# Kernel tuning notes

Hardware: AMD Instinct MI355X
Metric: run time of the kernel (lower is better)

## Reference

```python
import jax, jax.numpy as jnp
import numpy as np

N_EMBD = 1024
N_HEAD = 16
HEAD_DIM = N_EMBD // N_HEAD

def setup_inputs() -> dict:
    key = jax.random.key(0)
    ks = jax.random.split(key, 5)
    B, T, C = 2, 2048, N_EMBD
    s = 1.0 / np.sqrt(C)
    x = jax.random.normal(ks[0], (B, T, C), dtype=jnp.float32)
    W_qkv = jax.random.normal(ks[1], (C, 3 * C), dtype=jnp.float32) * s
    b_qkv = jax.random.normal(ks[2], (3 * C,), dtype=jnp.float32) * 0.02
    W_o = jax.random.normal(ks[3], (C, C), dtype=jnp.float32) * s
    b_o = jax.random.normal(ks[4], (C,), dtype=jnp.float32) * 0.02
    return {"x": x, "W_qkv": W_qkv, "b_qkv": b_qkv, "W_o": W_o, "b_o": b_o}

def reference(x, W_qkv, b_qkv, W_o, b_o):
    B, T, C = x.shape
    H, D = N_HEAD, HEAD_DIM
    scale = 1.0 / np.sqrt(D)
    qkv = jnp.einsum('btc,cf->btf', x, W_qkv) + b_qkv  # [B,T,3C]
    q, k, v = jnp.split(qkv, 3, axis=-1)
    # [B,H,T,D]
    q = q.reshape(B, T, H, D).transpose(0, 2, 1, 3)
    k = k.reshape(B, T, H, D).transpose(0, 2, 1, 3)
    v = v.reshape(B, T, H, D).transpose(0, 2, 1, 3)
    att = jnp.einsum('bhqd,bhkd->bhqk', q, k) * scale  # [B,H,T,T]
    causal = jnp.tril(jnp.ones((T, T), dtype=bool))
    att = jnp.where(causal[None, None], att, -jnp.inf)
    att = jax.nn.softmax(att, axis=-1)
    y = jnp.einsum('bhqk,bhkd->bhqd', att, v)  # [B,H,T,D]
    y = y.transpose(0, 2, 1, 3).reshape(B, T, C)
    return jnp.einsum('btc,cf->btf', y, W_o) + b_o
```

## Files before the change

### kernel.cpp

```cpp
#include <hip/hip_runtime.h>
#include <hip/hip_bf16.h>

#define TT 2048
#define BB 2
#define CC 1024
#define NH 16
#define HD 64

typedef __attribute__((ext_vector_type(8))) short short8;
typedef __attribute__((ext_vector_type(4))) short short4b;
typedef __attribute__((ext_vector_type(4))) float f32x4;

typedef unsigned int __attribute__((address_space(1))) ui_gas;
typedef unsigned int __attribute__((address_space(3))) ui_las;

#if __has_builtin(__builtin_amdgcn_mfma_f32_16x16x16bf16_1k)
#define PV16 1
#define VSS 4
#else
#define PV16 0
#define VSS 8
#endif

__device__ __forceinline__ float us2f(unsigned short u) {
    union { unsigned int i; float f; } v; v.i = ((unsigned int)u) << 16; return v.f;
}
__device__ __forceinline__ unsigned short f2us(float f) {
    union { float f; unsigned int i; } v; v.f = f;
    unsigned int i = v.i;
    unsigned int lsb = (i >> 16) & 1u;
    i += 0x7fffu + lsb;
    return (unsigned short)(i >> 16);
}
__device__ __forceinline__ unsigned int pack2_trunc(float a, float b) {
    union { float f; unsigned int u; } x, y; x.f = a; y.f = b;
    return (y.u & 0xffff0000u) | (x.u >> 16);
}

__device__ __forceinline__ void gl_lds16(const unsigned short* g, unsigned short* l) {
    __builtin_amdgcn_global_load_lds((const ui_gas*)g, (ui_las*)l, 16, 0, 0);
}

__device__ __forceinline__ float4 load4(const void* p, size_t i, int isbf) {
    if (isbf) {
        ushort4 u = *reinterpret_cast<const ushort4*>((const unsigned short*)p + i);
        return make_float4(us2f(u.x), us2f(u.y), us2f(u.z), us2f(u.w));
    } else {
        return *reinterpret_cast<const float4*>((const float*)p + i);
    }
}
__device__ __forceinline__ float load1(const void* p, size_t i, int isbf) {
    return isbf ? us2f(((const unsigned short*)p)[i]) : ((const float*)p)[i];
}

__global__ __launch_bounds__(256) void prep_kernel(
    const void* __restrict__ x, const void* __restrict__ Wqkv, const void* __restrict__ Wo,
    const void* __restrict__ bqkv, const void* __restrict__ bo,
    unsigned short* __restrict__ xb, unsigned short* __restrict__ Wqkvt,
    unsigned short* __restrict__ Wot, int* __restrict__ flags)
{
    __shared__ float Ls[64 * 65];
    __shared__ int sh_isbf;
    const int t = threadIdx.x;
    const int bid = blockIdx.x;

    const void* src;
    int mode, sub;
    if (bid < 2048)      { mode = 0; sub = bid;        src = x; }
    else if (bid < 2816) { mode = 1; sub = bid - 2048; src = Wqkv; }
    else                 { mode = 2; sub = bid - 2816; src = Wo; }

    if (bid == 0 && t < 64) {
        const void* ps[5] = {x, Wqkv, bqkv, Wo, bo};
        for (int k = 0; k < 5; ++k) {
            const unsigned short* u = (const unsigned short*)ps[k];
            int bad = 0;
            #pragma unroll
            for (int j = 0; j < 4; ++j) {
                float v = us2f(u[t * 4 + j]);
                if (!(fabsf(v) < 1e4f)) bad = 1;
            }
            unsigned long long m = __ballot(bad != 0);
            if (t == 0) flags[k] = (__popcll(m) < 4) ? 1 : 0;
        }
    }
    if (t < 64) {
        const unsigned short* u = (const unsigned short*)src;
        int bad = 0;
        #pragma unroll
        for (int j = 0; j < 4; ++j) {
            float v = us2f(u[t * 4 + j]);
            if (!(fabsf(v) < 1e4f)) bad = 1;
        }
        unsigned long long m = __ballot(bad != 0);
        if (t == 0) sh_isbf = (__popcll(m) < 4) ? 1 : 0;
    }
    __syncthreads();
    const int isbf = sh_isbf;

    if (mode == 0) {
        const size_t i = ((size_t)sub * 256 + t) * 8;
        float4 a = load4(src, i, isbf);
        float4 b = load4(src, i + 4, isbf);
        alignas(16) unsigned short pk[8];
        pk[0] = f2us(a.x); pk[1] = f2us(a.y); pk[2] = f2us(a.z); pk[3] = f2us(a.w);
        pk[4] = f2us(b.x); pk[5] = f2us(b.y); pk[6] = f2us(b.z); pk[7] = f2us(b.w);
        *reinterpret_cast<uint4*>(xb + i) = *reinterpret_cast<const uint4*>(pk);
        return;
    }

    int N, Krows, n0, k0;
    unsigned short* dst;
    if (mode == 1) { N = 3 * CC; Krows = CC; dst = Wqkvt; n0 = (sub % 48) * 64; k0 = (sub / 48) * 64; }
    else           { N = CC;     Krows = CC; dst = Wot;   n0 = (sub % 16) * 64; k0 = (sub / 16) * 64; }
    {
        const int r = t >> 2, cq = (t & 3) << 4;
        #pragma unroll
        for (int i = 0; i < 4; ++i) {
            float4 v = load4(src, (size_t)(k0 + r) * N + n0 + cq + i * 4, isbf);
            Ls[r * 65 + cq + i * 4 + 0] = v.x;
            Ls[r * 65 + cq + i * 4 + 1] = v.y;
            Ls[r * 65 + cq + i * 4 + 2] = v.z;
            Ls[r * 65 + cq + i * 4 + 3] = v.w;
        }
    }
    __syncthreads();
    {
        const int c = t & 63, kg = (t >> 6) * 16;
        alignas(16) unsigned short pk[16];
        #pragma unroll
        for (int i = 0; i < 16; ++i) pk[i] = f2us(Ls[(kg + i) * 65 + c]);
        unsigned short* d = dst + (size_t)(n0 + c) * Krows + k0 + kg;
        *reinterpret_cast<uint4*>(d + 0) = *reinterpret_cast<const uint4*>(&pk[0]);
        *reinterpret_cast<uint4*>(d + 8) = *reinterpret_cast<const uint4*>(&pk[8]);
    }
}

template<int WM, int WN, int NWM, int NWN, int SWZ, bool VTE>
__global__ __launch_bounds__(256) void gemm_mfma(
    const unsigned short* __restrict__ A,
    const unsigned short* __restrict__ Bt,
    const void* __restrict__ bias, void* __restrict__ C,
    unsigned short* __restrict__ Vt,
    int M, int N, int K,
    const int* __restrict__ flags, int biasfi, int cfi)
{
    constexpr int BM = WM * 16 * NWM, BN = WN * 16 * NWN;
    constexpr int ASL = BM / 16, BSL = BN / 16;
    constexpr int TOT = ASL + BSL;
    constexpr int PW  = TOT / 4;

    __shared__ __align__(16) unsigned short SH[3][TOT * 512];

    const int tid = threadIdx.x;
    const int l  = tid & 63;
    const int w  = tid >> 6;
    const int wm = w / NWN, wn = w % NWN;
    const int lm = l & 15;
    const int lk = (l >> 4) * 8;
    const int quad = l >> 4;

    int bx, by;
    if constexpr (SWZ == 1) {
        const int lin = blockIdx.y * 24 + blockIdx.x;
        const int xcd = lin & 7, loc = lin >> 3;
        bx = (xcd & 1) * 12 + loc % 12;
        by = (xcd >> 1) * 8 + loc / 12;
    } else if constexpr (SWZ == 2) {
        const int lin = blockIdx.y * 16 + blockIdx.x;
        const int xcd = lin & 7, loc = lin >> 3;
        bx = (xcd & 1) * 8 + (loc & 7);
        by = (xcd >> 1) * 16 + (loc >> 3);
    } else {
        bx = blockIdx.x; by = blockIdx.y;
    }
    const int bm = by * BM, bn = bx * BN;

    f32x4 acc[WM][WN];
    #pragma unroll
    for (int i = 0; i < WM; ++i)
        #pragma unroll
        for (int j = 0; j < WN; ++j) acc[i][j] = (f32x4){0.f, 0.f, 0.f, 0.f};

    auto stage = [&](int bb, int k0) {
        #pragma unroll
        for (int s = 0; s < PW; ++s) {
            const int slab = w * PW + s;
            const unsigned short* src;
            if (slab < ASL) src = A  + (size_t)(bm + slab * 16 + lm) * K + k0 + lk;
            else            src = Bt + (size_t)(bn + (slab - ASL) * 16 + lm) * K + k0 + lk;
            gl_lds16(src, &SH[bb][slab * 512]);
        }
    };

    auto compute = [&](int bb) {
        short8 af[WM], bf[WN];
        #pragma unroll
        for (int i = 0; i < WM; ++i)
            af[i] = *reinterpret_cast<const short8*>(&SH[bb][(wm * WM + i) * 512 + l * 8]);
        #pragma unroll
        for (int j = 0; j < WN; ++j)
            bf[j] = *reinterpret_cast<const short8*>(&SH[bb][(ASL + wn * WN + j) * 512 + l * 8]);
        #pragma unroll
        for (int i = 0; i < WM; ++i)
            #pragma unroll
            for (int j = 0; j < WN; ++j)
                acc[i][j] = __builtin_amdgcn_mfma_f32_16x16x32_bf16(af[i], bf[j], acc[i][j], 0, 0, 0);
    };

    const int nt = K >> 5;
    stage(0, 0);
    stage(1, 32);
    asm volatile("s_waitcnt vmcnt(%0)" :: "n"(PW) : "memory");
    __builtin_amdgcn_sched_barrier(0);
    __builtin_amdgcn_s_barrier();

    for (int t = 0; t < nt; ++t) {
        if (t + 2 < nt) stage((t + 2) % 3, (t + 2) << 5);
        compute(t % 3);
        if (t + 2 < nt) {
            asm volatile("s_waitcnt vmcnt(%0)" :: "n"(PW) : "memory");
        } else {
            asm volatile("s_waitcnt vmcnt(0)" ::: "memory");
        }
        __builtin_amdgcn_sched_barrier(0);
        __builtin_amdgcn_s_barrier();
    }

    const int bias_bf = (biasfi >= 0) ? flags[biasfi] : 0;
    const int c_bf    = (cfi >= 0) ? flags[cfi] : ((cfi == -2) ? 1 : 0);
    float bv[WN];
    #pragma unroll
    for (int j = 0; j < WN; ++j) bv[j] = load1(bias, bn + (WN * wn + j) * 16 + lm, bias_bf);

    constexpr int TS = BM + 8;
    unsigned short* FL = &SH[0][0];
    const bool vblk = VTE && (bn >= 2 * CC);

    #pragma unroll
    for (int i = 0; i < WM; ++i) {
        #pragma unroll
        for (int r = 0; r < 4; ++r) {
            const int rl = (WM * wm + i) * 16 + quad * 4 + r;
            const int row = bm + rl;
            #pragma unroll
            for (int j = 0; j < WN; ++j) {
                const int cl2 = (WN * wn + j) * 16 + lm;
                const int col = bn + cl2;
                const float val = acc[i][j][r] + bv[j];
                if (c_bf) {
                    const unsigned short us = f2us(val);
                    ((unsigned short*)C)[(size_t)row * N + col] = us;
                    if (vblk) FL[cl2 * TS + rl] = us;
                } else {
                    ((float*)C)[(size_t)row * N + col] = val;
                }
            }
        }
    }

    if constexpr (VTE) {
        static_assert(!VTE || (BM == 128 && BN % 64 == 0), "VTE geometry");
        static_assert(!VTE || (BN * (BM + 8) <= 3 * TOT * 512), "VTE LDS overlay");
        if (vblk) {
            __syncthreads();
            const int cl = tid >> 1, rq = tid & 1;
            const int cc2 = bn - 2 * CC + cl;
            const int hh = cc2 >> 6, dd = cc2 & 63;
            const int bq = bm >> 11;
            const int tk = (bm & (TT - 1)) + rq * 64;
            unsigned short* dst = Vt + ((size_t)(bq * NH + hh) * HD + dd) * TT + tk;
            const unsigned short* srcp = &FL[cl * TS + rq * 64];
            #pragma unroll
            for (int k = 0; k < 8; ++k)
                *(uint4*)(dst + k * 8) = *(const uint4*)(srcp + k * 8);
        }
    }
}

__global__ __launch_bounds__(256) void attn_mfma(
    const unsigned short* __restrict__ qkv,
    const unsigned short* __restrict__ Vt,
    unsigned short* __restrict__ y)
{
    __shared__ __align__(16) unsigned short Ksh[8 * 512];
    __shared__ __align__(16) unsigned short Vsh[1039 * VSS];

    const int tid = threadIdx.x;
    const int l   = tid & 63;
    const int w   = tid >> 6;
    const int quad = l >> 4;
    const int col  = l & 15;

    const int n  = blockIdx.x;
    const int g  = n >> 3;
    const int bh = (n & 7) * 4 + (g & 3);
    const int i  = g >> 2;
    const int tA = i, tB = 31 - i;
    const int b  = bh >> 4, h = bh & 15;

#if !PV16
    for (int ss = tid; ss < 1039; ss += 256)
        *(uint2*)(&Vsh[ss * 8 + 4]) = make_uint2(0u, 0u);
#endif

    const float QSCALE = 0.18033688f;
    short8 qfA[2], qfB[2];
    #pragma unroll
    for (int t2 = 0; t2 < 2; ++t2) {
        const int qt = t2 ? tB : tA;
        short8* qf = t2 ? qfB : qfA;
        const int token = qt * 64 + w * 16 + col;
        const unsigned short* qrow = qkv + (size_t)(b * TT + token) * 3 * CC + h * HD;
        #pragma unroll
        for (int ks = 0; ks < 2; ++ks) {
            ushort4 u0 = *(const ushort4*)(qrow + ks * 32 + quad * 8);
            ushort4 u1 = *(const ushort4*)(qrow + ks * 32 + quad * 8 + 4);
            alignas(16) unsigned short pk[8];
            pk[0] = f2us(us2f(u0.x) * QSCALE);
            pk[1] = f2us(us2f(u0.y) * QSCALE);
            pk[2] = f2us(us2f(u0.z) * QSCALE);
            pk[3] = f2us(us2f(u0.w) * QSCALE);
            pk[4] = f2us(us2f(u1.x) * QSCALE);
            pk[5] = f2us(us2f(u1.y) * QSCALE);
            pk[6] = f2us(us2f(u1.z) * QSCALE);
            pk[7] = f2us(us2f(u1.w) * QSCALE);
            qf[ks] = *(const short8*)pk;
        }
    }

    f32x4 oA[4], oB[4];
    #pragma unroll
    for (int nb = 0; nb < 4; ++nb) {
        oA[nb] = (f32x4){0.f, 0.f, 0.f, 0.f};
        oB[nb] = (f32x4){0.f, 0.f, 0.f, 0.f};
    }
    float lAc = 0.f, lBc = 0.f;

    const unsigned short* kbase = qkv + (size_t)b * TT * 3 * CC + CC + h * HD;
    const unsigned short* vbase = Vt + (size_t)bh * HD * TT;

    const int vd = tid >> 2, vg0 = (tid & 3) * 4;

    uint4 rk[2], rv[2];
    auto issue_loads = [&](int kt) {
        const unsigned short* ksrc = kbase + (size_t)(kt * 64 + l) * 3 * CC;
        #pragma unroll
        for (int c2 = 0; c2 < 2; ++c2) {
            const int c = 2 * w + c2;
            rk[c2] = *(const uint4*)(ksrc + c * 8);
        }
        const unsigned short* vsrc = vbase + (size_t)vd * TT + kt * 64 + vg0 * 4;
        rv[0] = *(const uint4*)(vsrc + 0);
        rv[1] = *(const uint4*)(vsrc + 8);
    };
    auto write_lds = [&]() {
        #pragma unroll
        for (int c2 = 0; c2 < 2; ++c2) {
            const int c = 2 * w + c2;
            const int ks = c >> 2, q = c & 3;
            const int slot = ((quad * 2 + ks) * 64 + q * 16 + col) * 8;
            *(uint4*)(&Ksh[slot]) = rk[c2];
        }
        *(uint2*)(&Vsh[((vg0 + 0) * 65 + vd) * VSS]) = make_uint2(rv[0].x, rv[0].y);
        *(uint2*)(&Vsh[((vg0 + 1) * 65 + vd) * VSS]) = make_uint2(rv[0].z, rv[0].w);
        *(uint2*)(&Vsh[((vg0 + 2) * 65 + vd) * VSS]) = make_uint2(rv[1].x, rv[1].y);
        *(uint2*)(&Vsh[((vg0 + 3) * 65 + vd) * VSS]) = make_uint2(rv[1].z, rv[1].w);
    };

    auto step = [&](const short8* qf, f32x4* o, float& l_i, bool diag) {
        f32x4 st[4];
        #pragma unroll
        for (int nb = 0; nb < 4; ++nb) {
            f32x4 acc = {0.f, 0.f, 0.f, 0.f};
            #pragma unroll
            for (int ks = 0; ks < 2; ++ks) {
                short8 kf = *(const short8*)(&Ksh[((nb * 2 + ks) * 64 + l) * 8]);
                acc = __builtin_amdgcn_mfma_f32_16x16x32_bf16(kf, qf[ks], acc, 0, 0, 0);
            }
            st[nb] = acc;
        }
        float pv[4][4];
        float rs = 0.f;
        #pragma unroll
        for (int nb = 0; nb < 4; ++nb)
            #pragma unroll
            for (int r = 0; r < 4; ++r) {
                float v = st[nb][r];
                if (diag && (nb * 16 + quad * 4 + r > w * 16 + col)) v = -3e38f;
                float p = __builtin_exp2f(v);
                pv[nb][r] = p;
                rs += p;
            }
        rs += __shfl_xor(rs, 16);
        rs += __shfl_xor(rs, 32);
        l_i += rs;
#if PV16
        short4b pf[4];
        #pragma unroll
        for (int nbk = 0; nbk < 4; ++nbk) {
            union { short4b s; unsigned int u[2]; } pk;
            pk.u[0] = pack2_trunc(pv[nbk][0], pv[nbk][1]);
            pk.u[1] = pack2_trunc(pv[nbk][2], pv[nbk][3]);
            pf[nbk] = pk.s;
        }
        #pragma unroll
        for (int nbd = 0; nbd < 4; ++nbd)
            #pragma unroll
            for (int nbk = 0; nbk < 4; ++nbk) {
                short4b vf = *(const short4b*)(&Vsh[((nbk * 4 + quad) * 65 + nbd * 16 + col) * VSS]);
                o[nbd] = __builtin_amdgcn_mfma_f32_16x16x16bf16_1k(pf[nbk], vf, o[nbd], 0, 0, 0);
            }
#else
        short8 pf[4];
        #pragma unroll
        for (int nbk = 0; nbk < 4; ++nbk) {
            union { short8 s; unsigned int u[4]; } pk;
            pk.u[0] = pack2_trunc(pv[nbk][0], pv[nbk][1]);
            pk.u[1] = pack2_trunc(pv[nbk][2], pv[nbk][3]);
            pk.u[2] = 0u; pk.u[3] = 0u;
            pf[nbk] = pk.s;
        }
        #pragma unroll
        for (int nbd = 0; nbd < 4; ++nbd)
            #pragma unroll
            for (int nbk = 0; nbk < 4; ++nbk) {
                short8 vf = *(const short8*)(&Vsh[((nbk * 4 + quad) * 65 + nbd * 16 + col) * VSS]);
                o[nbd] = __builtin_amdgcn_mfma_f32_16x16x32_bf16(pf[nbk], vf, o[nbd], 0, 0, 0);
            }
#endif
    };

    issue_loads(0);
    for (int kt = 0; kt <= tB; ++kt) {
        write_lds();
        __syncthreads();
        if (kt < tB) issue_loads(kt + 1);
        step(qfB, oB, lBc, kt == tB);
        if (kt <= tA) step(qfA, oA, lAc, kt == tA);
        __syncthreads();
    }

    #pragma unroll
    for (int t2 = 0; t2 < 2; ++t2) {
        const int qt = t2 ? tB : tA;
        f32x4* o = t2 ? oB : oA;
        const float inv = 1.f / (t2 ? lBc : lAc);
        float invr[4];
        #pragma unroll
        for (int r = 0; r < 4; ++r) invr[r] = __shfl(inv, quad * 4 + r);
        #pragma unroll
        for (int nb = 0; nb < 4; ++nb)
            #pragma unroll
            for (int r = 0; r < 4; ++r) {
                int token = qt * 64 + w * 16 + quad * 4 + r;
                y[(size_t)(b * TT + token) * CC + h * HD + nb * 16 + col] = f2us(o[nb][r] * invr[r]);
            }
    }
}

extern "C" void kernel_launch(void* const* d_in, const int* in_sizes, int n_in,
                              void* d_out, int out_size, void* d_ws, size_t ws_size,
                              hipStream_t stream) {
    const int M = BB * TT;

    char* ws = (char*)d_ws;
    int*            flags = (int*)ws;                         ws += 256;
    unsigned short* xb    = (unsigned short*)ws;              ws += (size_t)M * CC * 2;
    unsigned short* Wqkvt = (unsigned short*)ws;              ws += (size_t)3 * CC * CC * 2;
    unsigned short* Wot   = (unsigned short*)ws;              ws += (size_t)CC * CC * 2;
    unsigned short* qkv   = (unsigned short*)ws;              ws += (size_t)M * 3 * CC * 2;
    unsigned short* Vt    = (unsigned short*)ws;              ws += (size_t)BB * NH * HD * TT * 2;
    unsigned short* y     = (unsigned short*)ws;

    prep_kernel<<<3072, 256, 0, stream>>>(d_in[0], d_in[1], d_in[3], d_in[2], d_in[4],
                                          xb, Wqkvt, Wot, flags);

    gemm_mfma<4, 4, 2, 2, 1, true><<<dim3(3 * CC / 128, M / 128), 256, 0, stream>>>(
        xb, Wqkvt, d_in[2], qkv, Vt, M, 3 * CC, CC, flags, 2, -2);

    attn_mfma<<<512, 256, 0, stream>>>(qkv, Vt, y);

    gemm_mfma<2, 2, 2, 2, 2, false><<<dim3(CC / 64, M / 64), 256, 0, stream>>>(
        y, Wot, d_in[4], d_out, nullptr, M, CC, CC, flags, 4, 0);
}
```

Measured before the change: 233.2 us.

## Add dedicated 256x192 QKV GEMM kernel and enlarge output-projection tiles

Introduces a specialized 512-thread QKV projection kernel with 256x192 block tiles and 8 waves: four waves load A and four load B, each wave computes an 8x3 MFMA grid. It keeps the triple-buffered LDS pipeline, the XCD-aware block swizzle and the fused V-transpose epilogue, now handling tiles that straddle the V boundary. The output projection switches from 64x64 to 128x128 tiles with a new swizzle. Larger tiles aim to raise operand reuse and cut redundant global loads, at the cost of fewer blocks (256 and 256) and higher register pressure.

```diff
diff --git a/kernel.cpp b/kernel.cpp
--- a/kernel.cpp
+++ b/kernel.cpp
@@ -133,6 +133,134 @@
         unsigned short* d = dst + (size_t)(n0 + c) * Krows + k0 + kg;
         *reinterpret_cast<uint4*>(d + 0) = *reinterpret_cast<const uint4*>(&pk[0]);
         *reinterpret_cast<uint4*>(d + 8) = *reinterpret_cast<const uint4*>(&pk[8]);
+    }
+}
+
+__global__ __launch_bounds__(512, 2) void gemm_qkv(
+    const unsigned short* __restrict__ A,
+    const unsigned short* __restrict__ Bt,
+    const void* __restrict__ bias, unsigned short* __restrict__ Cq,
+    unsigned short* __restrict__ Vt, const int* __restrict__ flags)
+{
+    constexpr int K = CC;
+    constexpr int QBM = 256, QBN = 192;
+    constexpr int ASL = QBM / 16;
+    constexpr int TOT = ASL + QBN / 16;
+    constexpr int TS  = QBM + 8;
+    __shared__ __align__(16) unsigned short SH[QBN * TS];
+
+    const int tid = threadIdx.x;
+    const int l = tid & 63, w = tid >> 6;
+    const int wm = w >> 2, wn = w & 3;
+    const int lm = l & 15, lk = (l >> 4) * 8, quad = l >> 4;
+
+    const int lin = blockIdx.y * 16 + blockIdx.x;
+    const int xcd = lin & 7, loc = lin >> 3;
+    const int bx = (xcd & 3) * 4 + (loc & 3);
+    const int by = (xcd >> 2) * 8 + (loc >> 2);
+    const int bm = by * QBM, bn = bx * QBN;
+
+    f32x4 acc[8][3];
+    #pragma unroll
+    for (int i = 0; i < 8; ++i)
+        #pragma unroll
+        for (int j = 0; j < 3; ++j) acc[i][j] = (f32x4){0.f, 0.f, 0.f, 0.f};
+
+    auto stage = [&](int bb, int k0) {
+        unsigned short* base = SH + bb * (TOT * 512);
+        if (w < 4) {
+            #pragma unroll
+            for (int s = 0; s < 4; ++s) {
+                const int slab = w * 4 + s;
+                gl_lds16(A + (size_t)(bm + slab * 16 + lm) * K + k0 + lk,
+                         base + slab * 512);
+            }
+        } else {
+            #pragma unroll
+            for (int s = 0; s < 3; ++s) {
+                const int slab = ASL + (w - 4) * 3 + s;
+                gl_lds16(Bt + (size_t)(bn + (slab - ASL) * 16 + lm) * K + k0 + lk,
+                         base + slab * 512);
+            }
+        }
+    };
+
+    auto compute = [&](int bb) {
+        const unsigned short* base = SH + bb * (TOT * 512);
+        short8 af[8], bf[3];
+        #pragma unroll
+        for (int i = 0; i < 8; ++i)
+            af[i] = *reinterpret_cast<const short8*>(&base[(wm * 8 + i) * 512 + l * 8]);
+        #pragma unroll
+        for (int j = 0; j < 3; ++j)
+            bf[j] = *reinterpret_cast<const short8*>(&base[(ASL + wn * 3 + j) * 512 + l * 8]);
+        #pragma unroll
+        for (int i = 0; i < 8; ++i)
+            #pragma unroll
+            for (int j = 0; j < 3; ++j)
+                acc[i][j] = __builtin_amdgcn_mfma_f32_16x16x32_bf16(af[i], bf[j], acc[i][j], 0, 0, 0);
+    };
+
+    const int nt = K >> 5;
+    stage(0, 0);
+    stage(1, 32);
+    if (w < 4) asm volatile("s_waitcnt vmcnt(4)" ::: "memory");
+    else       asm volatile("s_waitcnt vmcnt(3)" ::: "memory");
+    __builtin_amdgcn_sched_barrier(0);
+    __builtin_amdgcn_s_barrier();
+
+    for (int t = 0; t < nt; ++t) {
+        if (t + 2 < nt) stage((t + 2) % 3, (t + 2) << 5);
+        compute(t % 3);
+        if (t + 2 < nt) {
+            if (w < 4) asm volatile("s_waitcnt vmcnt(4)" ::: "memory");
+            else       asm volatile("s_waitcnt vmcnt(3)" ::: "memory");
+        } else {
+            asm volatile("s_waitcnt vmcnt(0)" ::: "memory");
+        }
+        __builtin_amdgcn_sched_barrier(0);
+        __builtin_amdgcn_s_barrier();
+    }
+
+    const int bias_bf = flags[2];
+    float bv[3];
+    #pragma unroll
+    for (int j = 0; j < 3; ++j) bv[j] = load1(bias, bn + (wn * 3 + j) * 16 + lm, bias_bf);
+
+    const int vstart = 2 * CC - bn;
+
+    #pragma unroll
+    for (int i = 0; i < 8; ++i) {
+        #pragma unroll
+        for (int r = 0; r < 4; ++r) {
+            const int rl = wm * 128 + i * 16 + quad * 4 + r;
+            const int row = bm + rl;
+            #pragma unroll
+            for (int j = 0; j < 3; ++j) {
+                const int cl2 = (wn * 3 + j) * 16 + lm;
+                const unsigned short us = f2us(acc[i][j][r] + bv[j]);
+                Cq[(size_t)row * (3 * CC) + bn + cl2] = us;
+                if (cl2 >= vstart) SH[cl2 * TS + rl] = us;
+            }
+        }
+    }
+
+    if (vstart < QBN) {
+        __syncthreads();
+        const int v0 = vstart > 0 ? vstart : 0;
+        const int vcnt = QBN - v0;
+        if (tid < vcnt * 2) {
+            const int cl = v0 + (tid >> 1), rq = tid & 1;
+            const int cc2 = bn + cl - 2 * CC;
+            const int hh = cc2 >> 6, dd = cc2 & 63;
+            const int bq = bm >> 11;
+            const int tk = (bm & (TT - 1)) + rq * 128;
+            unsigned short* dst = Vt + ((size_t)(bq * NH + hh) * HD + dd) * TT + tk;
+            const unsigned short* srcp = &SH[cl * TS + rq * 128];
+            #pragma unroll
+            for (int k = 0; k < 16; ++k)
+                *(uint4*)(dst + k * 8) = *(const uint4*)(srcp + k * 8);
+        }
     }
 }
 
@@ -161,16 +289,11 @@
     const int quad = l >> 4;
 
     int bx, by;
-    if constexpr (SWZ == 1) {
-        const int lin = blockIdx.y * 24 + blockIdx.x;
+    if constexpr (SWZ == 4) {
+        const int lin = blockIdx.y * 8 + blockIdx.x;
         const int xcd = lin & 7, loc = lin >> 3;
-        bx = (xcd & 1) * 12 + loc % 12;
-        by = (xcd >> 1) * 8 + loc / 12;
-    } else if constexpr (SWZ == 2) {
-        const int lin = blockIdx.y * 16 + blockIdx.x;
-        const int xcd = lin & 7, loc = lin >> 3;
-        bx = (xcd & 1) * 8 + (loc & 7);
-        by = (xcd >> 1) * 16 + (loc >> 3);
+        bx = loc & 7;
+        by = xcd * 4 + (loc >> 3);
     } else {
         bx = blockIdx.x; by = blockIdx.y;
     }
@@ -233,47 +356,18 @@
     #pragma unroll
     for (int j = 0; j < WN; ++j) bv[j] = load1(bias, bn + (WN * wn + j) * 16 + lm, bias_bf);
 
-    constexpr int TS = BM + 8;
-    unsigned short* FL = &SH[0][0];
-    const bool vblk = VTE && (bn >= 2 * CC);
-
     #pragma unroll
     for (int i = 0; i < WM; ++i) {
         #pragma unroll
         for (int r = 0; r < 4; ++r) {
-            const int rl = (WM * wm + i) * 16 + quad * 4 + r;
-            const int row = bm + rl;
+            const int row = bm + (WM * wm + i) * 16 + quad * 4 + r;
             #pragma unroll
             for (int j = 0; j < WN; ++j) {
-                const int cl2 = (WN * wn + j) * 16 + lm;
-                const int col = bn + cl2;
+                const int col = bn + (WN * wn + j) * 16 + lm;
                 const float val = acc[i][j][r] + bv[j];
-                if (c_bf) {
-                    const unsigned short us = f2us(val);
-                    ((unsigned short*)C)[(size_t)row * N + col] = us;
-                    if (vblk) FL[cl2 * TS + rl] = us;
-                } else {
-                    ((float*)C)[(size_t)row * N + col] = val;
-                }
-            }
-        }
-    }
-
-    if constexpr (VTE) {
-        static_assert(!VTE || (BM == 128 && BN % 64 == 0), "VTE geometry");
-        static_assert(!VTE || (BN * (BM + 8) <= 3 * TOT * 512), "VTE LDS overlay");
-        if (vblk) {
-            __syncthreads();
-            const int cl = tid >> 1, rq = tid & 1;
-            const int cc2 = bn - 2 * CC + cl;
-            const int hh = cc2 >> 6, dd = cc2 & 63;
-            const int bq = bm >> 11;
-            const int tk = (bm & (TT - 1)) + rq * 64;
-            unsigned short* dst = Vt + ((size_t)(bq * NH + hh) * HD + dd) * TT + tk;
-            const unsigned short* srcp = &FL[cl * TS + rq * 64];
-            #pragma unroll
-            for (int k = 0; k < 8; ++k)
-                *(uint4*)(dst + k * 8) = *(const uint4*)(srcp + k * 8);
+                if (c_bf) ((unsigned short*)C)[(size_t)row * N + col] = f2us(val);
+                else      ((float*)C)[(size_t)row * N + col] = val;
+            }
         }
     }
 }
@@ -476,11 +570,10 @@
     prep_kernel<<<3072, 256, 0, stream>>>(d_in[0], d_in[1], d_in[3], d_in[2], d_in[4],
                                           xb, Wqkvt, Wot, flags);
 
-    gemm_mfma<4, 4, 2, 2, 1, true><<<dim3(3 * CC / 128, M / 128), 256, 0, stream>>>(
-        xb, Wqkvt, d_in[2], qkv, Vt, M, 3 * CC, CC, flags, 2, -2);
+    gemm_qkv<<<dim3(16, 16), 512, 0, stream>>>(xb, Wqkvt, d_in[2], qkv, Vt, flags);
 
     attn_mfma<<<512, 256, 0, stream>>>(qkv, Vt, y);
 
-    gemm_mfma<2, 2, 2, 2, 2, false><<<dim3(CC / 64, M / 64), 256, 0, stream>>>(
+    gemm_mfma<4, 4, 2, 2, 4, false><<<dim3(CC / 128, M / 128), 256, 0, stream>>>(
         y, Wot, d_in[4], d_out, nullptr, M, CC, CC, flags, 4, 0);
 }
```

Result: faster. 206.4 us (-11.5%).
